# Optimization experiments

Measured on AMD Instinct MI355X. Metric: run time of the kernel, lower is better.

The kernel has to match this reference:

```python
import jax, jax.numpy as jnp
import numpy as np

D_MODEL = 1024
D_STATE = 16
D_CONV = 4
EXPAND = 2
D_INNER = EXPAND * D_MODEL          # 2048
DT_RANK = (D_MODEL + 15) // 16      # 64
B_SZ, SEQ = 2, 1024
LN_EPS = 1e-6


def setup_inputs() -> dict:
    key = jax.random.key(0)
    ks = jax.random.split(key, 12)
    s = 0.02
    x = jax.random.normal(ks[0], (B_SZ, SEQ, D_MODEL), dtype=jnp.float32)
    W_in = jax.random.normal(ks[1], (D_MODEL, 2 * D_INNER), dtype=jnp.float32) * s
    conv_w = jax.random.normal(ks[2], (D_INNER, D_CONV), dtype=jnp.float32) * s
    conv_b = jnp.zeros((D_INNER,), dtype=jnp.float32)
    W_xproj = jax.random.normal(ks[3], (D_INNER, DT_RANK + 2 * D_STATE), dtype=jnp.float32) * s
    W_dt = jax.random.normal(ks[4], (DT_RANK, D_INNER), dtype=jnp.float32) * (DT_RANK ** -0.5)
    # dt bias ~ log-uniform init as in Mamba (softplus^-1 of dt in [1e-3, 1e-1])
    dt = jnp.exp(jax.random.uniform(ks[5], (D_INNER,)) * (np.log(0.1) - np.log(1e-3)) + np.log(1e-3))
    b_dt = dt + jnp.log(-jnp.expm1(-dt))  # inverse softplus
    A_log = jnp.log(jnp.broadcast_to(jnp.arange(1, D_STATE + 1, dtype=jnp.float32), (D_INNER, D_STATE)))
    D_param = jnp.ones((D_INNER,), dtype=jnp.float32)
    W_out = jax.random.normal(ks[6], (D_INNER, D_MODEL), dtype=jnp.float32) * s
    gamma = jnp.ones((D_MODEL,), dtype=jnp.float32)
    beta = jnp.zeros((D_MODEL,), dtype=jnp.float32)
    return {"x": x, "W_in": W_in, "conv_w": conv_w, "conv_b": conv_b,
            "W_xproj": W_xproj, "W_dt": W_dt, "b_dt": b_dt, "A_log": A_log,
            "D_param": D_param, "W_out": W_out, "gamma": gamma, "beta": beta}


def _mamba(x, W_in, conv_w, conv_b, W_xproj, W_dt, b_dt, A_log, D_param, W_out):
    B, L, _ = x.shape
    xz = x @ W_in                                  # [B,L,2*d_inner]
    xi, z = jnp.split(xz, 2, axis=-1)              # [B,L,d_inner] each
    # causal depthwise conv1d, kernel D_CONV
    xp = jnp.pad(xi, ((0, 0), (D_CONV - 1, 0), (0, 0)))
    xc = conv_b
    for k in range(D_CONV):
        xc = xc + xp[:, k:k + L, :] * conv_w[:, k]
    xc = jax.nn.silu(xc)                           # [B,L,d_inner]
    x_dbl = xc @ W_xproj                           # [B,L,dt_rank+2*d_state]
    dt_r = x_dbl[..., :DT_RANK]
    B_ssm = x_dbl[..., DT_RANK:DT_RANK + D_STATE]  # [B,L,d_state]
    C_ssm = x_dbl[..., DT_RANK + D_STATE:]         # [B,L,d_state]
    dt = jax.nn.softplus(dt_r @ W_dt + b_dt)       # [B,L,d_inner]
    A = -jnp.exp(A_log)                            # [d_inner,d_state]
    dA = jnp.exp(dt[..., None] * A)                # [B,L,d_inner,d_state]
    dBu = dt[..., None] * B_ssm[:, :, None, :] * xc[..., None]
    # selective scan over time (time-major for lax.scan)
    dA_t = jnp.moveaxis(dA, 1, 0)                  # [L,B,d_inner,d_state]
    dBu_t = jnp.moveaxis(dBu, 1, 0)
    C_t = jnp.moveaxis(C_ssm, 1, 0)                # [L,B,d_state]
    h0 = jnp.zeros((B, D_INNER, D_STATE), dtype=x.dtype)

    def step(h, inp):
        a, bu, c = inp
        h = a * h + bu
        y = jnp.einsum('bdn,bn->bd', h, c)
        return h, y

    _, ys = jax.lax.scan(step, h0, (dA_t, dBu_t, C_t))
    y = jnp.moveaxis(ys, 0, 1)                     # [B,L,d_inner]
    y = y + xc * D_param
    y = y * jax.nn.silu(z)
    return y @ W_out                               # [B,L,d_model]


def reference(x, W_in, conv_w, conv_b, W_xproj, W_dt, b_dt, A_log, D_param, W_out, gamma, beta):
    m = _mamba(x, W_in, conv_w, conv_b, W_xproj, W_dt, b_dt, A_log, D_param, W_out)
    mu = jnp.mean(m, axis=-1, keepdims=True)
    var = jnp.mean(jnp.square(m - mu), axis=-1, keepdims=True)
    ln = (m - mu) * jax.lax.rsqrt(var + LN_EPS) * gamma + beta
    return x + ln
```

## Files before the change

### kernel.cpp

```cpp
#include <hip/hip_runtime.h>
#include <math.h>

#define DM   1024
#define DI   2048
#define DS   16
#define DTR  64
#define NB   2
#define SEQL 1024
#define NTOK (NB*SEQL)
#define XND  96
#define XNP  128
#define CK   128
#define CL   8

typedef __bf16 bf16x8 __attribute__((ext_vector_type(8)));
typedef __bf16 bf16x4 __attribute__((ext_vector_type(4)));
typedef float  f32x4  __attribute__((ext_vector_type(4)));

#define PREP_BLOCKS 3872

__device__ inline void trans_tile64(const float* __restrict__ W,
                                    __bf16* __restrict__ WT, int K, int N,
                                    int n0, int k0, int tid, __bf16 (*t)[65])
{
    const int tx = tid & 63, ty = tid >> 6;
    #pragma unroll
    for (int i = 0; i < 16; i++)
        t[ty * 16 + i][tx] = (__bf16)W[(size_t)(k0 + ty * 16 + i) * N + n0 + tx];
    __syncthreads();
    #pragma unroll
    for (int i = 0; i < 16; i++)
        WT[(size_t)(n0 + ty * 16 + i) * K + k0 + tx] = t[tx][ty * 16 + i];
}

__global__ __launch_bounds__(256) void prep(
    const float* __restrict__ x, const float* __restrict__ W_in,
    const float* __restrict__ W_out, const float* __restrict__ W_dt,
    const float* __restrict__ W_xprj,
    __bf16* __restrict__ xb, __bf16* __restrict__ W_inT,
    __bf16* __restrict__ W_outT, __bf16* __restrict__ WdtT,
    __bf16* __restrict__ W_xprT, float* __restrict__ xdbl)
{
    __shared__ __bf16 t[64][65];
    int bid = blockIdx.x;
    const int tid = threadIdx.x;

    if (bid < 256) {
        const int i = bid * 1024 + tid * 4;
        const float4 z = {0.f, 0.f, 0.f, 0.f};
        *reinterpret_cast<float4*>(&xdbl[i]) = z;
        return;
    }
    bid -= 256;
    if (bid < 1024) {
        const int e = (bid * 256 + tid) * 8;
        const float4 v0 = *reinterpret_cast<const float4*>(&x[e]);
        const float4 v1 = *reinterpret_cast<const float4*>(&x[e + 4]);
        bf16x8 o;
        o[0] = (__bf16)v0.x; o[1] = (__bf16)v0.y; o[2] = (__bf16)v0.z; o[3] = (__bf16)v0.w;
        o[4] = (__bf16)v1.x; o[5] = (__bf16)v1.y; o[6] = (__bf16)v1.z; o[7] = (__bf16)v1.w;
        *reinterpret_cast<bf16x8*>(&xb[e]) = o;
        return;
    }
    bid -= 1024;
    if (bid < 1024) {
        trans_tile64(W_in, W_inT, DM, 2 * DI, (bid & 63) * 64, (bid >> 6) * 64, tid, t);
        return;
    }
    bid -= 1024;
    if (bid < 512) {
        trans_tile64(W_out, W_outT, DI, DM, (bid & 15) * 64, (bid >> 4) * 64, tid, t);
        return;
    }
    bid -= 512;
    if (bid < 32) {
        trans_tile64(W_dt, WdtT, DTR, DI, bid * 64, 0, tid, t);
        return;
    }
    bid -= 32;
    {
        const int idx = bid * 256 + tid;
        const int k = idx & (DI - 1);
        const int n = idx >> 11;
        W_xprT[(size_t)n * DI + k] = (n < XND) ? (__bf16)W_xprj[(size_t)k * XND + n]
                                               : (__bf16)0.f;
    }
}

template<int MODE, int SWZ, int TN>
__global__ __launch_bounds__(256) void gemm_bf16(
    const __bf16* __restrict__ A, const __bf16* __restrict__ Bt,
    void* __restrict__ Cp, int M, int N, int K, int ldc,
    const float* __restrict__ bias)
{
    constexpr int NFR = TN / 32;
    __shared__ __bf16 smem[128 * 64 + TN * 64];
    __bf16* As = smem;
    __bf16* Bs = smem + 128 * 64;
    const int tid  = threadIdx.x;
    const int lane = tid & 63;
    const int wid  = tid >> 6;
    const int wr   = wid >> 1, wc = wid & 1;

    int bx = blockIdx.x, by = blockIdx.y;
    if (SWZ != 0) {
        const int gx = gridDim.x, gy = gridDim.y;
        const int nxy = gx * gy;
        const int q = nxy >> 3;
        int lin = by * gx + bx;
        lin = (lin & 7) * q + (lin >> 3);
        if (SWZ == 1) { by = lin / gx; bx = lin % gx; }
        else          { bx = lin / gy; by = lin % gy; }
    }
    const int brow = by * 128, bcol = bx * TN;
    const int kper = K / gridDim.z;
    const int kbeg = blockIdx.z * kper, kend = kbeg + kper;

    f32x4 acc[4][NFR] = {};

    for (int k0 = kbeg; k0 < kend; k0 += 64) {
        __syncthreads();
        if (MODE == 2) {
            const float* Af = reinterpret_cast<const float*>(A);
            #pragma unroll
            for (int p = 0; p < 4; p++) {
                const int i = p * 256 + tid;
                const int r = i >> 3;
                const int j = i & 7;
                const float4 v0 = *reinterpret_cast<const float4*>(
                    &Af[(size_t)(brow + r) * XNP + j * 8]);
                const float4 v1 = *reinterpret_cast<const float4*>(
                    &Af[(size_t)(brow + r) * XNP + j * 8 + 4]);
                bf16x8 o;
                o[0] = (__bf16)v0.x; o[1] = (__bf16)v0.y; o[2] = (__bf16)v0.z; o[3] = (__bf16)v0.w;
                o[4] = (__bf16)v1.x; o[5] = (__bf16)v1.y; o[6] = (__bf16)v1.z; o[7] = (__bf16)v1.w;
                *reinterpret_cast<bf16x8*>(&As[r * 64 + ((j ^ (r & 7))) * 8]) = o;
            }
        } else {
            #pragma unroll
            for (int p = 0; p < 4; p++) {
                const int i = p * 256 + tid;
                const int r = i >> 3;
                const int gc = ((i & 7) ^ (r & 7)) * 8;
                __builtin_amdgcn_global_load_lds(
                    (const __attribute__((address_space(1))) void*)(A + (size_t)(brow + r) * K + k0 + gc),
                    (__attribute__((address_space(3))) void*)(&As[i * 8]), 16, 0, 0);
            }
        }
        #pragma unroll
        for (int p = 0; p < TN / 32; p++) {
            const int i = p * 256 + tid;
            const int r = i >> 3;
            const int gc = ((i & 7) ^ (r & 7)) * 8;
            __builtin_amdgcn_global_load_lds(
                (const __attribute__((address_space(1))) void*)(Bt + (size_t)(bcol + r) * K + k0 + gc),
                (__attribute__((address_space(3))) void*)(&Bs[i * 8]), 16, 0, 0);
        }
        __syncthreads();
        bf16x8 a[2][4], b[2][NFR];
        const int rA = wr * 64 + (lane & 15);
        const int rB = wc * (TN / 2) + (lane & 15);
        const int cq = lane >> 4;
        const int rx = lane & 7;
        #pragma unroll
        for (int ks = 0; ks < 2; ks++) {
            const int sl = ((ks * 4 + cq) ^ rx) * 8;
            #pragma unroll
            for (int m = 0; m < 4; m++)
                a[ks][m] = *reinterpret_cast<const bf16x8*>(&As[(rA + m * 16) * 64 + sl]);
            #pragma unroll
            for (int n = 0; n < NFR; n++)
                b[ks][n] = *reinterpret_cast<const bf16x8*>(&Bs[(rB + n * 16) * 64 + sl]);
        }
        #pragma unroll
        for (int ks = 0; ks < 2; ks++)
            #pragma unroll
            for (int m = 0; m < 4; m++)
                #pragma unroll
                for (int n = 0; n < NFR; n++)
                    acc[m][n] = __builtin_amdgcn_mfma_f32_16x16x32_bf16(
                        a[ks][m], b[ks][n], acc[m][n], 0, 0, 0);
    }
    const int crl = wr * 64 + (lane >> 4) * 4;
    const int ccl = wc * (TN / 2) + (lane & 15);

    if (MODE == 1) {
        #pragma unroll
        for (int m = 0; m < 4; m++)
            #pragma unroll
            for (int n = 0; n < NFR; n++) {
                const int col = bcol + ccl + n * 16;
                #pragma unroll
                for (int j = 0; j < 4; j++)
                    atomicAdd(&((float*)Cp)[(size_t)(brow + crl + m * 16 + j) * ldc + col],
                              acc[m][n][j]);
            }
    } else {
        __syncthreads();
        __bf16* Cs = smem;
        #pragma unroll
        for (int m = 0; m < 4; m++)
            #pragma unroll
            for (int n = 0; n < NFR; n++) {
                #pragma unroll
                for (int j = 0; j < 4; j++) {
                    float v = acc[m][n][j];
                    if (MODE == 2) {
                        v += bias[bcol + ccl + n * 16];
                        v = fmaxf(v, 0.f) + log1pf(__expf(-fabsf(v)));
                    }
                    Cs[(crl + m * 16 + j) * TN + ccl + n * 16] = (__bf16)v;
                }
            }
        __syncthreads();
        __bf16* Cb = (__bf16*)Cp +
            (size_t)blockIdx.z * ((MODE == 3) ? (size_t)M * ldc : 0);
        constexpr int CHUNKS = 128 * TN / 8;
        #pragma unroll
        for (int p = 0; p < CHUNKS / 256; p++) {
            const int i = p * 256 + tid;
            const int r = i / (TN / 8);
            const int cc = (i % (TN / 8)) * 8;
            *reinterpret_cast<bf16x8*>(&Cb[(size_t)(brow + r) * ldc + bcol + cc]) =
                *reinterpret_cast<const bf16x8*>(&Cs[r * TN + cc]);
        }
    }
}

__global__ __launch_bounds__(256) void conv_silu(
    const __bf16* __restrict__ xzb, const float* __restrict__ conv_w,
    const float* __restrict__ conv_b, __bf16* __restrict__ xcb)
{
    const int g  = blockIdx.x * 256 + threadIdx.x;
    const int d0 = (g & 255) * 8;
    const int tok = g >> 8;
    const int t   = tok & (SEQL - 1);

    float4 wv[8];
    #pragma unroll
    for (int j = 0; j < 8; j++)
        wv[j] = *reinterpret_cast<const float4*>(&conv_w[(d0 + j) * 4]);
    float acc[8];
    {
        const float4 b0 = *reinterpret_cast<const float4*>(&conv_b[d0]);
        const float4 b1 = *reinterpret_cast<const float4*>(&conv_b[d0 + 4]);
        acc[0] = b0.x; acc[1] = b0.y; acc[2] = b0.z; acc[3] = b0.w;
        acc[4] = b1.x; acc[5] = b1.y; acc[6] = b1.z; acc[7] = b1.w;
    }
    #pragma unroll
    for (int k = 0; k < 4; k++) {
        const int tt = t + k - 3;
        if (tt >= 0) {
            const bf16x8 v = *reinterpret_cast<const bf16x8*>(
                &xzb[(size_t)(tok + k - 3) * (2 * DI) + d0]);
            #pragma unroll
            for (int j = 0; j < 8; j++) {
                const float wk = (k == 0) ? wv[j].x : (k == 1) ? wv[j].y
                               : (k == 2) ? wv[j].z : wv[j].w;
                acc[j] += (float)v[j] * wk;
            }
        }
    }
    bf16x8 o;
    #pragma unroll
    for (int j = 0; j < 8; j++) {
        const float a = acc[j];
        o[j] = (__bf16)(a / (1.f + __expf(-a)));
    }
    *reinterpret_cast<bf16x8*>(&xcb[(size_t)g * 8]) = o;
}

__global__ __launch_bounds__(256) void scan_partial(
    const __bf16* __restrict__ xcb, const float* __restrict__ xdbl,
    const __bf16* __restrict__ dtb, const float* __restrict__ A_log,
    __bf16* __restrict__ hpart, float* __restrict__ sdtb)
{
    __shared__ float Bsh[CL][16];
    const int tid = threadIdx.x;
    const int d = blockIdx.x * 256 + tid;
    const int c = blockIdx.y, b = blockIdx.z;
    const size_t base = (size_t)b * SEQL + c * CL;
    {
        const int st = tid >> 4, sg = tid & 15;
        if (st < CL) Bsh[st][sg] = xdbl[(base + st) * XNP + DTR + sg];
    }
    float dtv[CL], xcv[CL];
    #pragma unroll
    for (int t = 0; t < CL; t++) {
        dtv[t] = (float)dtb[(base + t) * DI + d];
        xcv[t] = (float)xcb[(base + t) * DI + d];
    }
    float Av[16];
    #pragma unroll
    for (int i = 0; i < 4; i++) {
        const float4 v = *reinterpret_cast<const float4*>(&A_log[(size_t)d * 16 + i * 4]);
        Av[i*4+0] = -__expf(v.x); Av[i*4+1] = -__expf(v.y);
        Av[i*4+2] = -__expf(v.z); Av[i*4+3] = -__expf(v.w);
    }
    __syncthreads();
    float h[16] = {};
    float sdt = 0.f;
    #pragma unroll
    for (int t = 0; t < CL; t++) {
        sdt += dtv[t];
        const float dx = dtv[t] * xcv[t];
        #pragma unroll
        for (int n = 0; n < 16; n++)
            h[n] = __expf(dtv[t] * Av[n]) * h[n] + dx * Bsh[t][n];
    }
    const size_t ob = ((size_t)(b * CK + c) * DI + d) * 16;
    bf16x8 o0, o1;
    #pragma unroll
    for (int i = 0; i < 8; i++) { o0[i] = (__bf16)h[i]; o1[i] = (__bf16)h[i + 8]; }
    *reinterpret_cast<bf16x8*>(&hpart[ob])     = o0;
    *reinterpret_cast<bf16x8*>(&hpart[ob + 8]) = o1;
    sdtb[(size_t)(b * CK + c) * DI + d] = sdt;
}

__global__ __launch_bounds__(256) void scan_combine(
    const float* __restrict__ A_log, const float* __restrict__ sdtb,
    const __bf16* __restrict__ hpart, __bf16* __restrict__ hentry)
{
    const int idx = blockIdx.x * 256 + threadIdx.x;
    const int n = idx & 15;
    const int d = (idx >> 4) & (DI - 1);
    const int b = idx >> 15;
    const float A = -__expf(A_log[(size_t)d * 16 + n]);
    float h = 0.f;
    for (int cb = 0; cb < CK / 16; cb++) {
        float hl[16], sv[16];
        #pragma unroll
        for (int j = 0; j < 16; j++) {
            const int c = cb * 16 + j;
            hl[j] = (float)hpart[((size_t)(b * CK + c) * DI + d) * 16 + n];
            sv[j] = sdtb[(size_t)(b * CK + c) * DI + d];
        }
        #pragma unroll
        for (int j = 0; j < 16; j++) {
            const int c = cb * 16 + j;
            hentry[((size_t)(b * CK + c) * DI + d) * 16 + n] = (__bf16)h;
            h = __expf(A * sv[j]) * h + hl[j];
        }
    }
}

__global__ __launch_bounds__(256) void scan_final(
    const __bf16* __restrict__ xzb, const __bf16* __restrict__ xcb,
    const float* __restrict__ xdbl, const __bf16* __restrict__ dtb,
    const float* __restrict__ A_log, const float* __restrict__ Dp,
    const __bf16* __restrict__ hentry, __bf16* __restrict__ yb)
{
    __shared__ float Bsh[CL][16];
    __shared__ float Csh[CL][16];
    const int tid = threadIdx.x;
    const int d = blockIdx.x * 256 + tid;
    const int c = blockIdx.y, b = blockIdx.z;
    const size_t base = (size_t)b * SEQL + c * CL;
    {
        const int st = tid >> 4, sg = tid & 15;
        if (st < CL)
            Bsh[st][sg] = xdbl[(base + st) * XNP + DTR + sg];
        else if (st < 2 * CL)
            Csh[st - CL][sg] = xdbl[(base + st - CL) * XNP + DTR + DS + sg];
    }
    float dtv[CL], xcv[CL], zv[CL];
    #pragma unroll
    for (int t = 0; t < CL; t++) {
        dtv[t] = (float)dtb[(base + t) * DI + d];
        xcv[t] = (float)xcb[(base + t) * DI + d];
        zv[t]  = (float)xzb[(base + t) * (2 * DI) + DI + d];
    }
    float Av[16];
    #pragma unroll
    for (int i = 0; i < 4; i++) {
        const float4 v = *reinterpret_cast<const float4*>(&A_log[(size_t)d * 16 + i * 4]);
        Av[i*4+0] = -__expf(v.x); Av[i*4+1] = -__expf(v.y);
        Av[i*4+2] = -__expf(v.z); Av[i*4+3] = -__expf(v.w);
    }
    float h[16];
    const size_t ob = ((size_t)(b * CK + c) * DI + d) * 16;
    {
        const bf16x8 v0 = *reinterpret_cast<const bf16x8*>(&hentry[ob]);
        const bf16x8 v1 = *reinterpret_cast<const bf16x8*>(&hentry[ob + 8]);
        #pragma unroll
        for (int i = 0; i < 8; i++) { h[i] = (float)v0[i]; h[i + 8] = (float)v1[i]; }
    }
    const float Dv = Dp[d];
    __syncthreads();
    #pragma unroll
    for (int t = 0; t < CL; t++) {
        const float dx = dtv[t] * xcv[t];
        float y = 0.f;
        #pragma unroll
        for (int n = 0; n < 16; n++) {
            h[n] = __expf(dtv[t] * Av[n]) * h[n] + dx * Bsh[t][n];
            y += h[n] * Csh[t][n];
        }
        y += xcv[t] * Dv;
        y *= zv[t] / (1.f + __expf(-zv[t]));
        yb[(base + t) * DI + d] = (__bf16)y;
    }
}

__global__ __launch_bounds__(256) void ln_add(
    const float* __restrict__ x, const __bf16* __restrict__ mpart,
    const float* __restrict__ gamma, const float* __restrict__ beta,
    float* __restrict__ out)
{
    const int tok = blockIdx.x;
    const int tid = threadIdx.x;
    const int lane = tid & 63, wave = tid >> 6;
    __shared__ float red[4];
    __shared__ float stats[2];

    float4 v = {0.f, 0.f, 0.f, 0.f};
    #pragma unroll
    for (int p = 0; p < 4; p++) {
        const bf16x4 mv = *reinterpret_cast<const bf16x4*>(
            &mpart[((size_t)p * NTOK + tok) * DM + tid * 4]);
        v.x += (float)mv[0]; v.y += (float)mv[1];
        v.z += (float)mv[2]; v.w += (float)mv[3];
    }
    float s = v.x + v.y + v.z + v.w;
    #pragma unroll
    for (int o = 32; o > 0; o >>= 1) s += __shfl_down(s, o, 64);
    if (lane == 0) red[wave] = s;
    __syncthreads();
    if (tid == 0) stats[0] = (red[0] + red[1] + red[2] + red[3]) * (1.f / DM);
    __syncthreads();
    const float mu = stats[0];
    const float dx = v.x - mu, dy = v.y - mu, dz = v.z - mu, dw = v.w - mu;
    float q = dx * dx + dy * dy + dz * dz + dw * dw;
    #pragma unroll
    for (int o = 32; o > 0; o >>= 1) q += __shfl_down(q, o, 64);
    if (lane == 0) red[wave] = q;
    __syncthreads();
    if (tid == 0)
        stats[1] = rsqrtf((red[0] + red[1] + red[2] + red[3]) * (1.f / DM) + 1e-6f);
    __syncthreads();
    const float rs = stats[1];

    const float4 g  = reinterpret_cast<const float4*>(gamma)[tid];
    const float4 bb = reinterpret_cast<const float4*>(beta)[tid];
    const float4 xv = reinterpret_cast<const float4*>(&x[(size_t)tok * DM])[tid];
    float4 o;
    o.x = xv.x + dx * rs * g.x + bb.x;
    o.y = xv.y + dy * rs * g.y + bb.y;
    o.z = xv.z + dz * rs * g.z + bb.z;
    o.w = xv.w + dw * rs * g.w + bb.w;
    reinterpret_cast<float4*>(&out[(size_t)tok * DM])[tid] = o;
}

extern "C" void kernel_launch(void* const* d_in, const int* in_sizes, int n_in,
                              void* d_out, int out_size, void* d_ws, size_t ws_size,
                              hipStream_t stream)
{
    const float* x      = (const float*)d_in[0];
    const float* W_in   = (const float*)d_in[1];
    const float* conv_w = (const float*)d_in[2];
    const float* conv_b = (const float*)d_in[3];
    const float* W_xprj = (const float*)d_in[4];
    const float* W_dt   = (const float*)d_in[5];
    const float* b_dt   = (const float*)d_in[6];
    const float* A_log  = (const float*)d_in[7];
    const float* D_par  = (const float*)d_in[8];
    const float* W_out  = (const float*)d_in[9];
    const float* gamma  = (const float*)d_in[10];
    const float* beta   = (const float*)d_in[11];
    float* out = (float*)d_out;

    char* w = (char*)d_ws;
    __bf16* xzb    = (__bf16*)(w + 0);
    __bf16* xcb    = (__bf16*)(w + 16777216);
    float*  xdbl   = (float*) (w + 25165824);
    __bf16* dtb    = (__bf16*)(w + 26214400);
    __bf16* mpart  = (__bf16*)(w + 34603008);
    __bf16* hpart  = (__bf16*)(w + 51380224);
    __bf16* hentry = (__bf16*)(w + 68157440);
    float*  sdtb   = (float*) (w + 84934656);
    __bf16* xb     = (__bf16*)(w + 87031808);
    __bf16* W_inT  = (__bf16*)(w + 91226112);
    __bf16* W_outT = (__bf16*)(w + 99614720);
    __bf16* W_xprT = (__bf16*)(w + 103809024);
    __bf16* WdtT   = (__bf16*)(w + 104333312);
    __bf16* yb     = (__bf16*)(w + 104595456);

    prep<<<PREP_BLOCKS, 256, 0, stream>>>(
        x, W_in, W_out, W_dt, W_xprj, xb, W_inT, W_outT, WdtT, W_xprT, xdbl);

    gemm_bf16<3, 2, 64><<<dim3(64, 16, 1), 256, 0, stream>>>(
        xb, W_inT, xzb, NTOK, 2 * DI, DM, 2 * DI, nullptr);

    conv_silu<<<(NTOK * DI / 8) / 256, 256, 0, stream>>>(xzb, conv_w, conv_b, xcb);

    gemm_bf16<1, 0, 128><<<dim3(1, 16, 16), 256, 0, stream>>>(
        xcb, W_xprT, xdbl, NTOK, XNP, DI, XNP, nullptr);

    gemm_bf16<2, 0, 64><<<dim3(32, 16, 1), 256, 0, stream>>>(
        (const __bf16*)xdbl, WdtT, dtb, NTOK, DI, DTR, DI, b_dt);

    scan_partial<<<dim3(DI / 256, CK, NB), 256, 0, stream>>>(
        xcb, xdbl, dtb, A_log, hpart, sdtb);
    scan_combine<<<NB * DI * DS / 256, 256, 0, stream>>>(A_log, sdtb, hpart, hentry);
    scan_final<<<dim3(DI / 256, CK, NB), 256, 0, stream>>>(
        xzb, xcb, xdbl, dtb, A_log, D_par, hentry, yb);

    gemm_bf16<3, 1, 64><<<dim3(16, 16, 4), 256, 0, stream>>>(
        yb, W_outT, mpart, NTOK, DM, DI, DM, nullptr);

    ln_add<<<NTOK, 256, 0, stream>>>(x, mpart, gamma, beta, out);
}
```

Before: 162.8 us.

## Double-buffer LDS tiles in bf16 GEMM to overlap global loads with MFMA

The bf16 GEMM now uses two LDS stages for the modes that load A via global_load_lds. The next K tile is issued before the current one is computed, with manual vmcnt waits and barriers. This is meant to hide global-to-LDS latency behind MFMA work. It doubles the shared memory per block, which may reduce occupancy. The fp32-A mode keeps the single-buffer path.

```diff
diff --git a/kernel.cpp b/kernel.cpp
--- a/kernel.cpp
+++ b/kernel.cpp
@@ -94,9 +94,11 @@
     const float* __restrict__ bias)
 {
     constexpr int NFR = TN / 32;
-    __shared__ __bf16 smem[128 * 64 + TN * 64];
-    __bf16* As = smem;
-    __bf16* Bs = smem + 128 * 64;
+    constexpr bool PIPE = (MODE != 2);
+    constexpr int ASZ = 128 * 64, BSZ = TN * 64;
+    constexpr int STG = (PIPE ? 2 : 1) * (ASZ + BSZ);
+    constexpr int SMEM = (STG > 128 * TN) ? STG : 128 * TN;
+    __shared__ __bf16 smem[SMEM];
     const int tid  = threadIdx.x;
     const int lane = tid & 63;
     const int wid  = tid >> 6;
@@ -118,8 +120,9 @@
 
     f32x4 acc[4][NFR] = {};
 
-    for (int k0 = kbeg; k0 < kend; k0 += 64) {
-        __syncthreads();
+    auto stage = [&](int buf, int k0) {
+        __bf16* As = smem + buf * (ASZ + BSZ);
+        __bf16* Bs = As + ASZ;
         if (MODE == 2) {
             const float* Af = reinterpret_cast<const float*>(A);
             #pragma unroll
@@ -156,7 +159,11 @@
                 (const __attribute__((address_space(1))) void*)(Bt + (size_t)(bcol + r) * K + k0 + gc),
                 (__attribute__((address_space(3))) void*)(&Bs[i * 8]), 16, 0, 0);
         }
-        __syncthreads();
+    };
+
+    auto compute = [&](int buf) {
+        const __bf16* As = smem + buf * (ASZ + BSZ);
+        const __bf16* Bs = As + ASZ;
         bf16x8 a[2][4], b[2][NFR];
         const int rA = wr * 64 + (lane & 15);
         const int rB = wc * (TN / 2) + (lane & 15);
@@ -180,7 +187,36 @@
                 for (int n = 0; n < NFR; n++)
                     acc[m][n] = __builtin_amdgcn_mfma_f32_16x16x32_bf16(
                         a[ks][m], b[ks][n], acc[m][n], 0, 0, 0);
-    }
+    };
+
+    const int nt = (kend - kbeg) >> 6;
+    if constexpr (PIPE) {
+        constexpr int LOADS = 4 + TN / 32;
+        stage(0, kbeg);
+        int cur = 0;
+        for (int t = 0; t < nt; t++) {
+            if (t + 1 < nt) {
+                stage(cur ^ 1, kbeg + ((t + 1) << 6));
+                asm volatile("s_waitcnt vmcnt(%0)" :: "n"(LOADS) : "memory");
+            } else {
+                asm volatile("s_waitcnt vmcnt(0)" ::: "memory");
+            }
+            __builtin_amdgcn_s_barrier();
+            __builtin_amdgcn_sched_barrier(0);
+            compute(cur);
+            __builtin_amdgcn_sched_barrier(0);
+            __builtin_amdgcn_s_barrier();
+            cur ^= 1;
+        }
+    } else {
+        for (int k0 = kbeg; k0 < kend; k0 += 64) {
+            __syncthreads();
+            stage(0, k0);
+            __syncthreads();
+            compute(0);
+        }
+    }
+
     const int crl = wr * 64 + (lane >> 4) * 4;
     const int ccl = wc * (TN / 2) + (lane & 15);
 
```

New measurement: 158.4 us. 2.7% less time.
